# Kernel optimization log

Measured on AMD Instinct MI355X. Metric: run time of the kernel, lower is better.

Reference implementation:

```python
import jax, jax.numpy as jnp
import numpy as np

B, S, D = 2, 2048, 768
H, DK, DV = 12, 64, 64


def setup_inputs() -> dict:
    key = jax.random.key(0)
    ks = jax.random.split(key, 12)
    sc = 0.02
    return {
        'q': jax.random.normal(ks[0], (B, S, D), jnp.float32),
        'k': jax.random.normal(ks[1], (B, S, D), jnp.float32),
        'v': jax.random.normal(ks[2], (B, S, D), jnp.float32),
        'mask': jnp.zeros((B, H, S, S), jnp.float32),
        'Wq': jax.random.normal(ks[3], (D, H * DK), jnp.float32) * sc,
        'bq': jnp.zeros((H * DK,), jnp.float32),
        'Wk': jax.random.normal(ks[4], (D, H * DK), jnp.float32) * sc,
        'bk': jnp.zeros((H * DK,), jnp.float32),
        'Wv': jax.random.normal(ks[5], (D, H * DV), jnp.float32) * sc,
        'bv': jnp.zeros((H * DV,), jnp.float32),
        'Wo': jax.random.normal(ks[6], (H * DV, D), jnp.float32) * sc,
        'bo': jnp.zeros((D,), jnp.float32),
    }


def reference(q, k, v, mask, Wq, bq, Wk, bk, Wv, bv, Wo, bo):
    b, s, _ = q.shape
    # projections -> [B, H, S, Dk/Dv]
    Q = (q @ Wq + bq).reshape(b, s, H, DK).transpose(0, 2, 1, 3)
    K = (k @ Wk + bk).reshape(b, s, H, DK).transpose(0, 2, 1, 3)
    V = (v @ Wv + bv).reshape(b, s, H, DV).transpose(0, 2, 1, 3)
    scale = 1.0 / np.sqrt(DK).astype(np.float32)
    scores = jnp.einsum('bhqd,bhkd->bhqk', Q, K) * scale + mask
    attn = jax.nn.softmax(scores, axis=-1)  # dropout rate 0.0 -> identity
    ctx = jnp.einsum('bhqk,bhkd->bhqd', attn, V)
    ctx = ctx.transpose(0, 2, 1, 3).reshape(b, s, H * DV)
    out = ctx @ Wo + bo
    return out, attn
```

## Files before the change

kernel.cpp:

```cpp
#include <hip/hip_runtime.h>
#include <hip/hip_bf16.h>

typedef unsigned short u16;
typedef __attribute__((ext_vector_type(8))) short s16x8;
typedef __attribute__((ext_vector_type(4))) float f32x4;

#define MFMA16(a, b, c) __builtin_amdgcn_mfma_f32_16x16x32_bf16((a), (b), (c), 0, 0, 0)

__device__ __forceinline__ float b2f(u16 u) {
    union { float f; unsigned int i; } c; c.i = ((unsigned int)u) << 16; return c.f;
}
__device__ __forceinline__ u16 f2b(float f) {
    union { float f; unsigned int i; } c; c.f = f;
    unsigned int i = c.i;
    return (u16)((i + 0x7fffu + ((i >> 16) & 1u)) >> 16);
}

__device__ __forceinline__ s16x8 load8b(const void* base, size_t idx, int isf32) {
    if (!isf32) {
        return *(const s16x8*)((const u16*)base + idx);
    } else {
        const float* p = (const float*)base + idx;
        f32x4 a = *(const f32x4*)p;
        f32x4 b = *(const f32x4*)(p + 4);
        s16x8 v;
        v[0] = (short)f2b(a[0]); v[1] = (short)f2b(a[1]);
        v[2] = (short)f2b(a[2]); v[3] = (short)f2b(a[3]);
        v[4] = (short)f2b(b[0]); v[5] = (short)f2b(b[1]);
        v[6] = (short)f2b(b[2]); v[7] = (short)f2b(b[3]);
        return v;
    }
}
__device__ __forceinline__ float loadsc(const void* base, size_t idx, int isf32) {
    return isf32 ? ((const float*)base)[idx] : b2f(((const u16*)base)[idx]);
}
__device__ __forceinline__ void load8f_nt(const void* base, size_t idx, int isf32, float* o) {
    if (!isf32) {
        s16x8 m = __builtin_nontemporal_load((const s16x8*)((const u16*)base + idx));
#pragma unroll
        for (int j = 0; j < 8; j++) o[j] = b2f((u16)m[j]);
    } else {
        const float* p = (const float*)base + idx;
        f32x4 a = __builtin_nontemporal_load((const f32x4*)p);
        f32x4 b = __builtin_nontemporal_load((const f32x4*)(p + 4));
        o[0] = a[0]; o[1] = a[1]; o[2] = a[2]; o[3] = a[3];
        o[4] = b[0]; o[5] = b[1]; o[6] = b[2]; o[7] = b[3];
    }
}

__global__ __launch_bounds__(64) void k_detect(const u16* __restrict__ q, int* __restrict__ flag) {
    int t = threadIdx.x;
    int cnt = 0;
#pragma unroll
    for (int i = 0; i < 16; i++) {
        u16 u = q[t * 16 + i];
        int e = (u >> 7) & 0xFF;
        cnt += (e >= 110 && e <= 135) ? 1 : 0;
    }
#pragma unroll
    for (int off = 32; off > 0; off >>= 1) cnt += __shfl_down(cnt, off);
    if (t == 0) *flag = (cnt < 850) ? 1 : 0;
}

__global__ __launch_bounds__(256) void k_cvt(
    const void* __restrict__ q, const void* __restrict__ k, const void* __restrict__ v,
    u16* __restrict__ Qc, u16* __restrict__ Kc, u16* __restrict__ Vc,
    const int* __restrict__ flag)
{
    const int isf32 = *flag;
    const int z = blockIdx.y;
    const void* src = (z == 0) ? q : (z == 1) ? k : v;
    u16* dst = (z == 0) ? Qc : (z == 1) ? Kc : Vc;
    size_t idx = ((size_t)blockIdx.x * 256 + threadIdx.x) * 8;
    s16x8 vv = load8b(src, idx, isf32);
    *(s16x8*)&dst[idx] = vv;
}

__global__ __launch_bounds__(256) void k_transpose(
    const void* __restrict__ w0, const void* __restrict__ w1,
    const void* __restrict__ w2, const void* __restrict__ w3,
    u16* __restrict__ wt, const int* __restrict__ flag)
{
    __shared__ __align__(16) u16 T[64 * 65];
    const int isf32 = *flag;
    const int z = blockIdx.z;
    const void* W = (z == 0) ? w0 : (z == 1) ? w1 : (z == 2) ? w2 : w3;
    u16* WT = wt + (size_t)z * 589824;
    const int n0 = blockIdx.x * 64, k0 = blockIdx.y * 64;
    const int t = threadIdx.x;
    const int r = t >> 3, c = (t & 7) * 8;
    for (int rr = r; rr < 64; rr += 32) {
        s16x8 v = load8b(W, (size_t)(k0 + rr) * 768 + n0 + c, isf32);
#pragma unroll
        for (int j = 0; j < 8; j++) T[(c + j) * 65 + rr] = (u16)v[j];
    }
    __syncthreads();
    const int n = t >> 3, kc = (t & 7) * 8;
    for (int nn = n; nn < 64; nn += 32) {
        s16x8 v;
#pragma unroll
        for (int j = 0; j < 8; j++) v[j] = (short)T[nn * 65 + kc + j];
        *(s16x8*)&WT[(size_t)(n0 + nn) * 768 + k0 + kc] = v;
    }
}

__device__ __forceinline__ void gemm_body(
    const void* __restrict__ A, int a_isf32, const u16* __restrict__ WT,
    const void* __restrict__ bias, int b_isf32, void* __restrict__ out,
    int out_isf32, int epi, int head, int m0)
{
    __shared__ __align__(16) u16 As[128 * 72];
    __shared__ __align__(16) u16 Bs[64 * 72];
    const int t = threadIdx.x;
    const int lane = t & 63, wave = t >> 6;
    const int quad = lane >> 4, l16 = lane & 15;
    const int mrow_base = (wave >> 1) * 64;
    const int ncol_base = (wave & 1) * 32;
    const int hbase = head * 64;

    f32x4 acc[4][2];
#pragma unroll
    for (int mt = 0; mt < 4; mt++)
#pragma unroll
        for (int nt = 0; nt < 2; nt++) acc[mt][nt] = (f32x4){0.f, 0.f, 0.f, 0.f};

    for (int k0 = 0; k0 < 768; k0 += 64) {
#pragma unroll
        for (int i = 0; i < 4; i++) {
            int seg = t + 256 * i;
            int r = seg >> 3, c = (seg & 7) * 8;
            *(s16x8*)&As[r * 72 + c] = load8b(A, (size_t)(m0 + r) * 768 + k0 + c, a_isf32);
        }
#pragma unroll
        for (int i = 0; i < 2; i++) {
            int seg = t + 256 * i;
            int r = seg >> 3, c = (seg & 7) * 8;
            *(s16x8*)&Bs[r * 72 + c] = *(const s16x8*)&WT[(size_t)(hbase + r) * 768 + k0 + c];
        }
        __syncthreads();
#pragma unroll
        for (int ks = 0; ks < 2; ks++) {
            s16x8 af[4], bf[2];
#pragma unroll
            for (int mt = 0; mt < 4; mt++)
                af[mt] = *(const s16x8*)&As[(mrow_base + mt * 16 + l16) * 72 + ks * 32 + quad * 8];
#pragma unroll
            for (int nt = 0; nt < 2; nt++)
                bf[nt] = *(const s16x8*)&Bs[(ncol_base + nt * 16 + l16) * 72 + ks * 32 + quad * 8];
#pragma unroll
            for (int mt = 0; mt < 4; mt++)
#pragma unroll
                for (int nt = 0; nt < 2; nt++)
                    acc[mt][nt] = MFMA16(af[mt], bf[nt], acc[mt][nt]);
        }
        __syncthreads();
    }

    if (epi == 2) {
#pragma unroll
        for (int mt = 0; mt < 4; mt++)
#pragma unroll
            for (int nt = 0; nt < 2; nt++) {
                int nc = ncol_base + nt * 16 + l16;
                float bvv = loadsc(bias, hbase + nc, b_isf32);
#pragma unroll
                for (int r = 0; r < 4; r++) {
                    int m = m0 + mrow_base + mt * 16 + quad * 4 + r;
                    float val = acc[mt][nt][r] + bvv;
                    size_t idx = (size_t)m * 768 + hbase + nc;
                    if (out_isf32) ((float*)out)[idx] = val;
                    else           ((u16*)out)[idx] = f2b(val);
                }
            }
    } else if (epi == 0) {
        u16* ob = (u16*)out;
#pragma unroll
        for (int mt = 0; mt < 4; mt++)
#pragma unroll
            for (int nt = 0; nt < 2; nt++) {
                int nc = ncol_base + nt * 16 + l16;
                float bvv = loadsc(bias, hbase + nc, b_isf32);
#pragma unroll
                for (int r = 0; r < 4; r++) {
                    int m = m0 + mrow_base + mt * 16 + quad * 4 + r;
                    int bidx = m >> 11, s = m & 2047;
                    ob[(((size_t)bidx * 12 + head) * 2048 + s) * 64 + nc] =
                        f2b(acc[mt][nt][r] + bvv);
                }
            }
    } else {
        u16* ob = (u16*)out;
        u16* Ts = As;
#pragma unroll
        for (int mt = 0; mt < 4; mt++)
#pragma unroll
            for (int nt = 0; nt < 2; nt++) {
                int nc = ncol_base + nt * 16 + l16;
                float bvv = loadsc(bias, hbase + nc, b_isf32);
#pragma unroll
                for (int r = 0; r < 4; r++) {
                    int ml = mrow_base + mt * 16 + quad * 4 + r;
                    Ts[nc * 136 + ml] = f2b(acc[mt][nt][r] + bvv);
                }
            }
        __syncthreads();
        const int bidx = m0 >> 11, sbase = m0 & 2047;
#pragma unroll
        for (int i = 0; i < 4; i++) {
            int seg = t + 256 * i;
            int dv = seg >> 4, scc = (seg & 15) * 8;
            s16x8 vv = *(const s16x8*)&Ts[dv * 136 + scc];
            *(s16x8*)&ob[(((size_t)bidx * 12 + head) * 64 + dv) * 2048 + sbase + scc] = vv;
        }
    }
}

__global__ __launch_bounds__(256) void k_qkv(
    const void* __restrict__ q, const void* __restrict__ k, const void* __restrict__ v,
    const u16* __restrict__ wt,
    const void* __restrict__ bq, const void* __restrict__ bk, const void* __restrict__ bv,
    u16* __restrict__ Q, u16* __restrict__ K, u16* __restrict__ Vt,
    const int* __restrict__ flag, int use_cvt)
{
    const int isf32 = *flag;
    const int z = blockIdx.z;
    const void* A = (z == 0) ? q : (z == 1) ? k : v;
    const u16* WTz = wt + (size_t)z * 589824;
    const void* bias = (z == 0) ? bq : (z == 1) ? bk : bv;
    u16* out = (z == 0) ? Q : (z == 1) ? K : Vt;
    gemm_body(A, use_cvt ? 0 : isf32, WTz, bias, isf32, out, 0,
              (z == 2) ? 1 : 0, blockIdx.y, blockIdx.x * 128);
}

__global__ __launch_bounds__(256) void k_oproj(
    const u16* __restrict__ ctx, const u16* __restrict__ wto,
    const void* __restrict__ bo, void* __restrict__ out,
    const int* __restrict__ flag)
{
    const int isf32 = *flag;
    gemm_body(ctx, 0, wto, bo, isf32, out, isf32, 2, blockIdx.y, blockIdx.x * 128);
}

__device__ __forceinline__ int sw_off(int row, int col) {
    int unit = col >> 3;
    int slot = (unit + row) & 7;
    return row * 2048 + (((unit & ~7) | slot) << 3) + (col & 7);
}

__global__ __launch_bounds__(512, 4) void k_attn(
    const u16* __restrict__ Q, const u16* __restrict__ K,
    const u16* __restrict__ Vt, const void* __restrict__ mask,
    void* __restrict__ outbase, u16* __restrict__ ctx,
    const int* __restrict__ flag)
{
    __shared__ __align__(16) u16 sc[16 * 2048];
    __shared__ __align__(16) float part[1024];
    __shared__ float invs[16];
    const int isf32 = *flag;
    const int t = threadIdx.x;
    const int lane = t & 63, wave = t >> 6;
    const int quad = lane >> 4, l16 = lane & 15;
    const int q0 = blockIdx.x * 16;
    const int h = blockIdx.y, b = blockIdx.z;
    const int bh = b * 12 + h;
    const size_t mrow0 = ((size_t)bh * 2048 + q0) * 2048;
    const int row = t >> 5, j32 = t & 31;

    float mk[8][8];
#pragma unroll
    for (int i = 0; i < 8; i++)
        load8f_nt(mask, mrow0 + (size_t)row * 2048 + j32 * 8 + i * 256, isf32, mk[i]);

    const u16* Qb = Q + ((size_t)bh * 2048 + q0) * 64;
    const s16x8 qf0 = *(const s16x8*)&Qb[l16 * 64 + quad * 8];
    const s16x8 qf1 = *(const s16x8*)&Qb[l16 * 64 + 32 + quad * 8];
    const u16* Kb = K + (size_t)bh * 2048 * 64;

#pragma unroll 4
    for (int it = 0; it < 16; it++) {
        const int kc = it * 128 + wave * 16;
        const u16* kp = &Kb[(size_t)(kc + l16) * 64 + quad * 8];
        s16x8 kf0 = *(const s16x8*)kp;
        s16x8 kf1 = *(const s16x8*)(kp + 32);
        f32x4 a = (f32x4){0.f, 0.f, 0.f, 0.f};
        a = MFMA16(qf0, kf0, a);
        a = MFMA16(qf1, kf1, a);
        const int col = kc + l16;
#pragma unroll
        for (int r = 0; r < 4; r++)
            sc[sw_off(quad * 4 + r, col)] = f2b(a[r] * 0.125f);
    }
    __syncthreads();

    float mx = -3.4e38f;
#pragma unroll
    for (int i = 0; i < 8; i++) {
        const int c0 = j32 * 8 + i * 256;
        s16x8 sv = *(const s16x8*)&sc[sw_off(row, c0)];
#pragma unroll
        for (int j = 0; j < 8; j++) {
            mk[i][j] += b2f((u16)sv[j]);
            mx = fmaxf(mx, mk[i][j]);
        }
    }
#pragma unroll
    for (int off = 16; off > 0; off >>= 1) mx = fmaxf(mx, __shfl_xor(mx, off));

    float sum = 0.f;
#pragma unroll
    for (int i = 0; i < 8; i++) {
        const int c0 = j32 * 8 + i * 256;
        s16x8 nv;
#pragma unroll
        for (int j = 0; j < 8; j++) {
            float e = __expf(mk[i][j] - mx);
            nv[j] = (short)f2b(e);
            sum += e;
        }
        *(s16x8*)&sc[sw_off(row, c0)] = nv;
    }
#pragma unroll
    for (int off = 16; off > 0; off >>= 1) sum += __shfl_xor(sum, off);
    const float inv = 1.0f / sum;
    if (j32 == 0) invs[row] = inv;
    __syncthreads();

    const int wg = wave >> 2;
    const int dv = (wave & 3) * 16 + l16;
    const u16* vrow = Vt + ((size_t)bh * 64 + dv) * 2048;
    f32x4 o = (f32x4){0.f, 0.f, 0.f, 0.f};
    const int kbase = wg * 32;
#pragma unroll 4
    for (int kk = 0; kk < 32; kk++) {
        const int kcol = (kbase + kk) * 32 + quad * 8;
        s16x8 pa = *(const s16x8*)&sc[sw_off(l16, kcol)];
        s16x8 vb = *(const s16x8*)&vrow[kcol];
        o = MFMA16(pa, vb, o);
    }
    if (wg == 1) *(f32x4*)&part[((wave & 3) * 64 + lane) * 4] = o;
    __syncthreads();
    if (wg == 0) {
        f32x4 o2 = *(const f32x4*)&part[((wave & 3) * 64 + lane) * 4];
#pragma unroll
        for (int r = 0; r < 4; r++) {
            float val = (o[r] + o2[r]) * invs[quad * 4 + r];
            ctx[((size_t)b * 2048 + q0 + quad * 4 + r) * 768 + h * 64 + dv] = f2b(val);
        }
    }

    const size_t aoff = 3145728 + mrow0 + (size_t)row * 2048;
#pragma unroll 2
    for (int i = 0; i < 8; i++) {
        const int c0 = j32 * 8 + i * 256;
        s16x8 sv = *(const s16x8*)&sc[sw_off(row, c0)];
        if (isf32) {
            float* arow = (float*)outbase + aoff;
            f32x4 lo, hi;
#pragma unroll
            for (int j = 0; j < 4; j++) lo[j] = b2f((u16)sv[j]) * inv;
#pragma unroll
            for (int j = 0; j < 4; j++) hi[j] = b2f((u16)sv[j + 4]) * inv;
            *(f32x4*)&arow[c0] = lo;
            *(f32x4*)&arow[c0 + 4] = hi;
        } else {
            u16* arow = (u16*)outbase + aoff;
            s16x8 pv;
#pragma unroll
            for (int j = 0; j < 8; j++) pv[j] = (short)f2b(b2f((u16)sv[j]) * inv);
            *(s16x8*)&arow[c0] = pv;
        }
    }
}

extern "C" void kernel_launch(void* const* d_in, const int* in_sizes, int n_in,
                              void* d_out, int out_size, void* d_ws, size_t ws_size,
                              hipStream_t stream) {
    const void* q    = d_in[0];
    const void* k    = d_in[1];
    const void* v    = d_in[2];
    const void* mask = d_in[3];
    const void* Wq   = d_in[4];
    const void* bq   = d_in[5];
    const void* Wk   = d_in[6];
    const void* bk   = d_in[7];
    const void* Wv   = d_in[8];
    const void* bv   = d_in[9];
    const void* Wo   = d_in[10];
    const void* bo   = d_in[11];

    u16* ws  = (u16*)d_ws;
    u16* WT  = ws;
    u16* Qb  = ws + 2359296;
    u16* Kb  = ws + 5505024;
    u16* Vtb = ws + 8650752;
    u16* ctx = ws + 11796480;
    int* flag = (int*)(ws + 14942208);

    u16* Qc = ws + 14942224;
    u16* Kc = Qc + 3145728;
    u16* Vc = Kc + 3145728;
    const int use_cvt = (ws_size >= (size_t)48758816) ? 1 : 0;

    k_detect<<<1, 64, 0, stream>>>((const u16*)q, flag);
    k_transpose<<<dim3(12, 12, 4), 256, 0, stream>>>(Wq, Wk, Wv, Wo, WT, flag);
    if (use_cvt) {
        k_cvt<<<dim3(1536, 3), 256, 0, stream>>>(q, k, v, Qc, Kc, Vc, flag);
        k_qkv<<<dim3(32, 12, 3), 256, 0, stream>>>(Qc, Kc, Vc, WT, bq, bk, bv,
                                                   Qb, Kb, Vtb, flag, 1);
    } else {
        k_qkv<<<dim3(32, 12, 3), 256, 0, stream>>>(q, k, v, WT, bq, bk, bv,
                                                   Qb, Kb, Vtb, flag, 0);
    }
    k_attn<<<dim3(128, 12, 2), 512, 0, stream>>>(Qb, Kb, Vtb, mask, d_out, ctx, flag);
    k_oproj<<<dim3(32, 12, 1), 256, 0, stream>>>(ctx, WT + 3 * 589824, bo, d_out, flag);
}
```

Before: 902.6 us.

## Double attention block to 1024 threads with one wave per softmax row

The attention kernel now runs 16 waves per block instead of 8. Each wave handles one query row in the softmax, and the PV product is split four ways along the key dimension, reduced through a larger shared partial buffer. The mask load moves from before the QK^T loop to inside the softmax loop, so it no longer overlaps with the score computation but needs fewer registers per thread. The aim is more parallelism and lower per-thread register pressure in this memory-bound kernel. The costs are a bigger partial-sum buffer, a longer final reduction, and possibly fewer resident blocks per CU.

```diff
diff --git a/kernel.cpp b/kernel.cpp
--- a/kernel.cpp
+++ b/kernel.cpp
@@ -247,14 +247,14 @@
     return row * 2048 + (((unit & ~7) | slot) << 3) + (col & 7);
 }
 
-__global__ __launch_bounds__(512, 4) void k_attn(
+__global__ __launch_bounds__(1024, 8) void k_attn(
     const u16* __restrict__ Q, const u16* __restrict__ K,
     const u16* __restrict__ Vt, const void* __restrict__ mask,
     void* __restrict__ outbase, u16* __restrict__ ctx,
     const int* __restrict__ flag)
 {
     __shared__ __align__(16) u16 sc[16 * 2048];
-    __shared__ __align__(16) float part[1024];
+    __shared__ __align__(16) float part[3072];
     __shared__ float invs[16];
     const int isf32 = *flag;
     const int t = threadIdx.x;
@@ -264,21 +264,15 @@
     const int h = blockIdx.y, b = blockIdx.z;
     const int bh = b * 12 + h;
     const size_t mrow0 = ((size_t)bh * 2048 + q0) * 2048;
-    const int row = t >> 5, j32 = t & 31;
-
-    float mk[8][8];
-#pragma unroll
-    for (int i = 0; i < 8; i++)
-        load8f_nt(mask, mrow0 + (size_t)row * 2048 + j32 * 8 + i * 256, isf32, mk[i]);
 
     const u16* Qb = Q + ((size_t)bh * 2048 + q0) * 64;
     const s16x8 qf0 = *(const s16x8*)&Qb[l16 * 64 + quad * 8];
     const s16x8 qf1 = *(const s16x8*)&Qb[l16 * 64 + 32 + quad * 8];
     const u16* Kb = K + (size_t)bh * 2048 * 64;
 
-#pragma unroll 4
-    for (int it = 0; it < 16; it++) {
-        const int kc = it * 128 + wave * 16;
+#pragma unroll
+    for (int it = 0; it < 8; it++) {
+        const int kc = it * 256 + wave * 16;
         const u16* kp = &Kb[(size_t)(kc + l16) * 64 + quad * 8];
         s16x8 kf0 = *(const s16x8*)kp;
         s16x8 kf1 = *(const s16x8*)(kp + 32);
@@ -292,10 +286,13 @@
     }
     __syncthreads();
 
+    const int row = wave;
+    float mk[4][8];
     float mx = -3.4e38f;
 #pragma unroll
-    for (int i = 0; i < 8; i++) {
-        const int c0 = j32 * 8 + i * 256;
+    for (int i = 0; i < 4; i++) {
+        const int c0 = lane * 8 + i * 512;
+        load8f_nt(mask, mrow0 + (size_t)row * 2048 + c0, isf32, mk[i]);
         s16x8 sv = *(const s16x8*)&sc[sw_off(row, c0)];
 #pragma unroll
         for (int j = 0; j < 8; j++) {
@@ -304,12 +301,12 @@
         }
     }
 #pragma unroll
-    for (int off = 16; off > 0; off >>= 1) mx = fmaxf(mx, __shfl_xor(mx, off));
+    for (int off = 32; off > 0; off >>= 1) mx = fmaxf(mx, __shfl_xor(mx, off));
 
     float sum = 0.f;
 #pragma unroll
-    for (int i = 0; i < 8; i++) {
-        const int c0 = j32 * 8 + i * 256;
+    for (int i = 0; i < 4; i++) {
+        const int c0 = lane * 8 + i * 512;
         s16x8 nv;
 #pragma unroll
         for (int j = 0; j < 8; j++) {
@@ -320,38 +317,43 @@
         *(s16x8*)&sc[sw_off(row, c0)] = nv;
     }
 #pragma unroll
-    for (int off = 16; off > 0; off >>= 1) sum += __shfl_xor(sum, off);
+    for (int off = 32; off > 0; off >>= 1) sum += __shfl_xor(sum, off);
     const float inv = 1.0f / sum;
-    if (j32 == 0) invs[row] = inv;
+    if (lane == 0) invs[row] = inv;
     __syncthreads();
 
-    const int wg = wave >> 2;
-    const int dv = (wave & 3) * 16 + l16;
+    const int wg = wave >> 2, dvq = wave & 3;
+    const int dv = dvq * 16 + l16;
     const u16* vrow = Vt + ((size_t)bh * 64 + dv) * 2048;
     f32x4 o = (f32x4){0.f, 0.f, 0.f, 0.f};
-    const int kbase = wg * 32;
 #pragma unroll 4
-    for (int kk = 0; kk < 32; kk++) {
-        const int kcol = (kbase + kk) * 32 + quad * 8;
+    for (int kk = 0; kk < 16; kk++) {
+        const int kcol = (wg * 16 + kk) * 32 + quad * 8;
         s16x8 pa = *(const s16x8*)&sc[sw_off(l16, kcol)];
         s16x8 vb = *(const s16x8*)&vrow[kcol];
         o = MFMA16(pa, vb, o);
     }
-    if (wg == 1) *(f32x4*)&part[((wave & 3) * 64 + lane) * 4] = o;
+    if (wg != 0) *(f32x4*)&part[(((wg - 1) * 4 + dvq) * 64 + lane) * 4] = o;
     __syncthreads();
     if (wg == 0) {
-        f32x4 o2 = *(const f32x4*)&part[((wave & 3) * 64 + lane) * 4];
+        f32x4 s = o;
+#pragma unroll
+        for (int j = 0; j < 3; j++) {
+            f32x4 p2 = *(const f32x4*)&part[((j * 4 + dvq) * 64 + lane) * 4];
+#pragma unroll
+            for (int r = 0; r < 4; r++) s[r] += p2[r];
+        }
 #pragma unroll
         for (int r = 0; r < 4; r++) {
-            float val = (o[r] + o2[r]) * invs[quad * 4 + r];
+            float val = s[r] * invs[quad * 4 + r];
             ctx[((size_t)b * 2048 + q0 + quad * 4 + r) * 768 + h * 64 + dv] = f2b(val);
         }
     }
 
     const size_t aoff = 3145728 + mrow0 + (size_t)row * 2048;
-#pragma unroll 2
-    for (int i = 0; i < 8; i++) {
-        const int c0 = j32 * 8 + i * 256;
+#pragma unroll
+    for (int i = 0; i < 4; i++) {
+        const int c0 = lane * 8 + i * 512;
         s16x8 sv = *(const s16x8*)&sc[sw_off(row, c0)];
         if (isf32) {
             float* arow = (float*)outbase + aoff;
@@ -411,6 +413,6 @@
         k_qkv<<<dim3(32, 12, 3), 256, 0, stream>>>(q, k, v, WT, bq, bk, bv,
                                                    Qb, Kb, Vtb, flag, 0);
     }
-    k_attn<<<dim3(128, 12, 2), 512, 0, stream>>>(Qb, Kb, Vtb, mask, d_out, ctx, flag);
+    k_attn<<<dim3(128, 12, 2), 1024, 0, stream>>>(Qb, Kb, Vtb, mask, d_out, ctx, flag);
     k_oproj<<<dim3(32, 12, 1), 256, 0, stream>>>(ctx, WT + 3 * 589824, bo, d_out, flag);
 }
```

After: 946.0 us. 1.05x slower.
